# Kernel optimization log

Measured on AMD Instinct MI355X. Metric: run time of the kernel, lower is better.

Reference implementation:

```python
import jax, jax.numpy as jnp
import numpy as np

N, E = 20000, 5000
IN_FT, OUT_FT = 128, 128
DENSITY = 0.01  # fraction of nonzeros in the incidence matrix


def setup_inputs() -> dict:
    key = jax.random.key(0)
    kx, kh, kw, kb = jax.random.split(key, 4)
    X = jax.random.normal(kx, (N, IN_FT), dtype=jnp.float32)
    H = (jax.random.uniform(kh, (N, E)) < DENSITY).astype(jnp.float32)
    # xavier_normal_ with gain=0.01
    xav_std = 0.01 * np.sqrt(2.0 / (IN_FT + OUT_FT))
    weight_trans = jax.random.normal(kw, (IN_FT, OUT_FT), dtype=jnp.float32) * xav_std
    bias = jax.random.normal(kb, (OUT_FT,), dtype=jnp.float32) * 0.01
    return {"X": X, "H": H, "weight_trans": weight_trans, "bias": bias}


def reference(X, H, weight_trans, bias):
    # X: [N, in_ft], H: [N, E] incidence
    Xw = X @ weight_trans                      # [N, out_ft]
    DV = jnp.sum(H, axis=1) + 1e-12            # node degrees, [N]
    DE = jnp.sum(H, axis=0) + 1e-12            # hyperedge degrees, [E]
    # G = diag(1/DV) @ H @ diag(1/DE) @ H^T applied to Xw, computed in the
    # efficient order without materializing the NxN matrix G:
    M = H.T @ Xw                               # [E, out_ft]
    M = M / DE[:, None]                        # diag(1/DE) scaling
    out = H @ M                                # [N, out_ft]
    out = out / DV[:, None]                    # diag(1/DV) scaling
    out = out + bias
    return jax.nn.relu(out)
```

## Files before the change

kernel.cpp:

```cpp
#include <hip/hip_runtime.h>
#include <hip/hip_bf16.h>

#define N_NODES 20000
#define N_EDGES 5000
#define FT 128
#define CH_ROWS 320
#define N_CHUNKS 63
#define N_PANELS 79
#define SEG 24
#define SEG_STRIDE 1536
#define MAX_DEG 320

__global__ __launch_bounds__(256) void x_to_bf16(
    const float2* __restrict__ X2, __hip_bfloat162* __restrict__ Xb2) {
  int i = blockIdx.x * 256 + threadIdx.x;
  Xb2[i] = __float22bfloat162_rn(X2[i]);
}

__global__ __launch_bounds__(256) void scan_cols(
    const float* __restrict__ H,
    int* __restrict__ seg,
    int* __restrict__ scnt,
    unsigned long long* __restrict__ Hbt) {
  const int wid = threadIdx.x >> 6, lane = threadIdx.x & 63;
  const int panel = (blockIdx.x % 20) * 4 + wid;
  const int chunk = blockIdx.x / 20;
  if (panel >= N_PANELS) return;
  const int c = panel * 64 + lane;
  const bool cvalid = c < N_EDGES;
  const int r0 = chunk * CH_ROWS;
  const int rend = min(r0 + CH_ROWS, N_NODES);

  int* myseg = seg + c * SEG_STRIDE + chunk * SEG;
  unsigned long long* hb = Hbt + (size_t)panel * N_NODES;
  int cnt = 0;
  unsigned long long msk = 0ull;

  for (int rb = r0; rb < rend; rb += 8) {
    float v[8];
    const float* base = H + (size_t)rb * N_EDGES + c;
#pragma unroll
    for (int k = 0; k < 8; ++k) v[k] = 0.f;
    if (cvalid) {
#pragma unroll
      for (int k = 0; k < 8; ++k) v[k] = base[(size_t)k * N_EDGES];
    }
#pragma unroll
    for (int k = 0; k < 8; ++k) {
      int r = rb + k;
      unsigned long long bal = __ballot(v[k] != 0.f);
      msk = ((r & 63) == lane) ? bal : msk;
      if (((r & 63) == 63) || (r == N_NODES - 1)) {
        int g0 = r & ~63;
        if (g0 + lane < N_NODES) hb[g0 + lane] = msk;
        msk = 0ull;
      }
      if (v[k] != 0.f) {
        if (cnt < SEG) myseg[cnt] = r;
        ++cnt;
      }
    }
  }
  if (cvalid) scnt[c * 64 + chunk] = (cnt > SEG) ? SEG : cnt;
}

__global__ __launch_bounds__(256) void edge_gather(
    const __hip_bfloat162* __restrict__ Xb2,
    const int* __restrict__ seg, const int* __restrict__ scnt,
    float2* __restrict__ P2, int* __restrict__ de) {
  __shared__ int sidx[4][MAX_DEG];
  const int wid = threadIdx.x >> 6, lane = threadIdx.x & 63;
  const int e = blockIdx.x * 4 + wid;

  int cl = (lane < N_CHUNKS) ? scnt[e * 64 + lane] : 0;
  cl = min(cl, SEG);
  int off = cl;
  for (int d = 1; d < 64; d <<= 1) {
    int t = __shfl_up(off, d);
    if (lane >= d) off += t;
  }
  int total = __shfl(off, 63);
  off -= cl;
  if (cl > 0) {
    const int* sb = seg + e * SEG_STRIDE + lane * SEG;
    for (int i = 0; i < cl; ++i) {
      int o = off + i;
      if (o < MAX_DEG) sidx[wid][o] = sb[i];
    }
  }
  __builtin_amdgcn_s_waitcnt(0);
  int t = min(total, MAX_DEG);

  float sx = 0.f, sy = 0.f;
  int g = 0;
  for (; g + 8 <= t; g += 8) {
    int n0 = sidx[wid][g + 0], n1 = sidx[wid][g + 1];
    int n2 = sidx[wid][g + 2], n3 = sidx[wid][g + 3];
    int n4 = sidx[wid][g + 4], n5 = sidx[wid][g + 5];
    int n6 = sidx[wid][g + 6], n7 = sidx[wid][g + 7];
    float2 a0 = __bfloat1622float2(Xb2[n0 * 64 + lane]);
    float2 a1 = __bfloat1622float2(Xb2[n1 * 64 + lane]);
    float2 a2 = __bfloat1622float2(Xb2[n2 * 64 + lane]);
    float2 a3 = __bfloat1622float2(Xb2[n3 * 64 + lane]);
    float2 a4 = __bfloat1622float2(Xb2[n4 * 64 + lane]);
    float2 a5 = __bfloat1622float2(Xb2[n5 * 64 + lane]);
    float2 a6 = __bfloat1622float2(Xb2[n6 * 64 + lane]);
    float2 a7 = __bfloat1622float2(Xb2[n7 * 64 + lane]);
    sx += (a0.x + a1.x) + (a2.x + a3.x) + (a4.x + a5.x) + (a6.x + a7.x);
    sy += (a0.y + a1.y) + (a2.y + a3.y) + (a4.y + a5.y) + (a6.y + a7.y);
  }
  for (; g < t; ++g) {
    float2 a = __bfloat1622float2(Xb2[sidx[wid][g] * 64 + lane]);
    sx += a.x; sy += a.y;
  }
  P2[e * 64 + lane] = make_float2(sx, sy);
  if (lane == 0) de[e] = total;
}

__global__ __launch_bounds__(256) void gemm_M(
    const float* __restrict__ P, const float* __restrict__ W,
    const int* __restrict__ de, float* __restrict__ M) {
  int f = threadIdx.x & (FT - 1);
  int half = threadIdx.x >> 7;
  int base = blockIdx.x * 16 + half * 8;
#pragma unroll
  for (int g = 0; g < 8; g += 4) {
    int e = base + g;
    if (e >= N_EDGES) break;
    const float* p0 = P + (e + 0) * FT;
    const float* p1 = P + (e + 1) * FT;
    const float* p2 = P + (e + 2) * FT;
    const float* p3 = P + (e + 3) * FT;
    float a0 = 0.f, a1 = 0.f, a2 = 0.f, a3 = 0.f;
#pragma unroll 4
    for (int k = 0; k < FT; ++k) {
      float w = W[k * FT + f];
      a0 += p0[k] * w; a1 += p1[k] * w; a2 += p2[k] * w; a3 += p3[k] * w;
    }
    M[(e + 0) * FT + f] = a0 / ((float)de[e + 0] + 1e-12f);
    M[(e + 1) * FT + f] = a1 / ((float)de[e + 1] + 1e-12f);
    M[(e + 2) * FT + f] = a2 / ((float)de[e + 2] + 1e-12f);
    M[(e + 3) * FT + f] = a3 / ((float)de[e + 3] + 1e-12f);
  }
}

__global__ __launch_bounds__(256) void row_apply(
    const unsigned long long* __restrict__ Hbt,
    const float2* __restrict__ M2,
    const float2* __restrict__ bias2,
    float2* __restrict__ out2) {
  const int wid = threadIdx.x >> 6, lane = threadIdx.x & 63;
  const int n = blockIdx.x * 4 + wid;

  unsigned long long m0 = Hbt[(size_t)lane * N_NODES + n];
  unsigned long long m1 = (lane < N_PANELS - 64)
      ? Hbt[(size_t)(64 + lane) * N_NODES + n] : 0ull;
  float sx = 0.f, sy = 0.f;
  int dv = 0;
  for (int p = 0; p < N_PANELS; ++p) {
    unsigned long long mp = (p < 64) ? __shfl(m0, p) : __shfl(m1, p - 64);
    if (mp == 0ull) continue;
    dv += __popcll(mp);
    int ebase = p * 64;
    while (mp) {
      int b = __ffsll(mp) - 1;
      mp &= mp - 1;
      float2 mv = M2[(ebase + b) * 64 + lane];
      sx += mv.x; sy += mv.y;
    }
  }
  float inv = 1.f / ((float)dv + 1e-12f);
  float2 bb = bias2[lane];
  float2 o;
  o.x = fmaxf(fmaf(sx, inv, bb.x), 0.f);
  o.y = fmaxf(fmaf(sy, inv, bb.y), 0.f);
  out2[n * 64 + lane] = o;
}

extern "C" void kernel_launch(void* const* d_in, const int* in_sizes, int n_in,
                              void* d_out, int out_size, void* d_ws, size_t ws_size,
                              hipStream_t stream) {
  const float* X    = (const float*)d_in[0];
  const float* H    = (const float*)d_in[1];
  const float* W    = (const float*)d_in[2];
  const float* bias = (const float*)d_in[3];
  float* out = (float*)d_out;

  int* ws = (int*)d_ws;
  int* seg                 = ws;
  int* scnt                = ws + 7766016;
  unsigned long long* Hbt  = (unsigned long long*)(ws + 8089600);
  __hip_bfloat162* Xb2     = (__hip_bfloat162*)(ws + 11249600);
  float* P                 = (float*)(ws + 12529600);
  int* de                  = ws + 13169600;
  float* M                 = (float*)(ws + 13174720);

  x_to_bf16 <<<5000, 256, 0, stream>>>((const float2*)X, Xb2);
  scan_cols <<<20 * N_CHUNKS, 256, 0, stream>>>(H, seg, scnt, Hbt);
  edge_gather<<<N_EDGES / 4, 256, 0, stream>>>(Xb2, seg, scnt, (float2*)P, de);
  gemm_M    <<<(N_EDGES + 15) / 16, 256, 0, stream>>>(P, W, de, M);
  row_apply <<<N_NODES / 4, 256, 0, stream>>>(Hbt, (const float2*)M,
                                              (const float2*)bias, (float2*)out);
}
```

Before: 690.3 us.

## Scan H row-wise into interleaved bitmask, then build per-edge lists from bitmask

Replaces the column-strided scan of the dense incidence matrix with a row-wise float4 scan that ballots each row into an 80-word bitmask, using an interleaved edge-to-bit mapping (edge = 256*(vp/4) + 4*lane + vp%4). A separate list_build kernel then reads the compact bitmask to produce per-edge node segments with 32 chunks instead of 63. row_apply reads node-major bitmask rows contiguously. The intent is to turn the 400MB H read into fully coalesced vector loads and decouple list building from that read, at the cost of an extra kernel and a second pass over the bitmask.

```diff
diff --git a/kernel.cpp b/kernel.cpp
--- a/kernel.cpp
+++ b/kernel.cpp
@@ -4,11 +4,11 @@
 #define N_NODES 20000
 #define N_EDGES 5000
 #define FT 128
-#define CH_ROWS 320
-#define N_CHUNKS 63
-#define N_PANELS 79
+#define NVP 80
+#define ROW_U64 80
+#define N_CHUNKS 32
+#define CH_ROWS 625
 #define SEG 24
-#define SEG_STRIDE 1536
 #define MAX_DEG 320
 
 __global__ __launch_bounds__(256) void x_to_bf16(
@@ -17,51 +17,59 @@
   Xb2[i] = __float22bfloat162_rn(X2[i]);
 }
 
-__global__ __launch_bounds__(256) void scan_cols(
-    const float* __restrict__ H,
+__global__ __launch_bounds__(256) void scan_rows(
+    const float4* __restrict__ H4, unsigned long long* __restrict__ Hbt) {
+  const int wid = threadIdx.x >> 6, lane = threadIdx.x & 63;
+  const int r = blockIdx.x * 4 + wid;
+  const float4* base = H4 + (size_t)r * 1250;
+  unsigned long long m_lo = 0ull, m_hi = 0ull;
+#pragma unroll 4
+  for (int g = 0; g < 20; ++g) {
+    int idx4 = g * 64 + lane;
+    float4 v = make_float4(0.f, 0.f, 0.f, 0.f);
+    if (idx4 < 1250) v = base[idx4];
+    unsigned long long b0 = __ballot(v.x != 0.f);
+    unsigned long long b1 = __ballot(v.y != 0.f);
+    unsigned long long b2 = __ballot(v.z != 0.f);
+    unsigned long long b3 = __ballot(v.w != 0.f);
+    int vp = 4 * g;
+    if (vp < 64) {
+      m_lo = (lane == vp)     ? b0 : m_lo;
+      m_lo = (lane == vp + 1) ? b1 : m_lo;
+      m_lo = (lane == vp + 2) ? b2 : m_lo;
+      m_lo = (lane == vp + 3) ? b3 : m_lo;
+    } else {
+      m_hi = (lane == vp - 64) ? b0 : m_hi;
+      m_hi = (lane == vp - 63) ? b1 : m_hi;
+      m_hi = (lane == vp - 62) ? b2 : m_hi;
+      m_hi = (lane == vp - 61) ? b3 : m_hi;
+    }
+  }
+  Hbt[(size_t)r * ROW_U64 + lane] = m_lo;
+  if (lane < 16) Hbt[(size_t)r * ROW_U64 + 64 + lane] = m_hi;
+}
+
+__global__ __launch_bounds__(256) void list_build(
+    const unsigned long long* __restrict__ Hbt,
     int* __restrict__ seg,
-    int* __restrict__ scnt,
-    unsigned long long* __restrict__ Hbt) {
-  const int wid = threadIdx.x >> 6, lane = threadIdx.x & 63;
-  const int panel = (blockIdx.x % 20) * 4 + wid;
-  const int chunk = blockIdx.x / 20;
-  if (panel >= N_PANELS) return;
-  const int c = panel * 64 + lane;
-  const bool cvalid = c < N_EDGES;
+    int* __restrict__ scnt) {
+  const int wid = threadIdx.x >> 6, lane = threadIdx.x & 63;
+  const int gw = blockIdx.x * 4 + wid;
+  const int vp = gw % NVP;
+  const int chunk = gw / NVP;
+  const int e = (vp >> 2) * 256 + 4 * lane + (vp & 3);
+  int* myseg = seg + e * (N_CHUNKS * SEG) + chunk * SEG;
   const int r0 = chunk * CH_ROWS;
-  const int rend = min(r0 + CH_ROWS, N_NODES);
-
-  int* myseg = seg + c * SEG_STRIDE + chunk * SEG;
-  unsigned long long* hb = Hbt + (size_t)panel * N_NODES;
   int cnt = 0;
-  unsigned long long msk = 0ull;
-
-  for (int rb = r0; rb < rend; rb += 8) {
-    float v[8];
-    const float* base = H + (size_t)rb * N_EDGES + c;
-#pragma unroll
-    for (int k = 0; k < 8; ++k) v[k] = 0.f;
-    if (cvalid) {
-#pragma unroll
-      for (int k = 0; k < 8; ++k) v[k] = base[(size_t)k * N_EDGES];
-    }
-#pragma unroll
-    for (int k = 0; k < 8; ++k) {
-      int r = rb + k;
-      unsigned long long bal = __ballot(v[k] != 0.f);
-      msk = ((r & 63) == lane) ? bal : msk;
-      if (((r & 63) == 63) || (r == N_NODES - 1)) {
-        int g0 = r & ~63;
-        if (g0 + lane < N_NODES) hb[g0 + lane] = msk;
-        msk = 0ull;
-      }
-      if (v[k] != 0.f) {
-        if (cnt < SEG) myseg[cnt] = r;
-        ++cnt;
-      }
-    }
-  }
-  if (cvalid) scnt[c * 64 + chunk] = (cnt > SEG) ? SEG : cnt;
+#pragma unroll 5
+  for (int i = 0; i < CH_ROWS; ++i) {
+    unsigned long long mp = Hbt[(size_t)(r0 + i) * ROW_U64 + vp];
+    if ((mp >> lane) & 1ull) {
+      if (cnt < SEG) myseg[cnt] = r0 + i;
+      ++cnt;
+    }
+  }
+  scnt[e * N_CHUNKS + chunk] = (cnt > SEG) ? SEG : cnt;
 }
 
 __global__ __launch_bounds__(256) void edge_gather(
@@ -72,17 +80,17 @@
   const int wid = threadIdx.x >> 6, lane = threadIdx.x & 63;
   const int e = blockIdx.x * 4 + wid;
 
-  int cl = (lane < N_CHUNKS) ? scnt[e * 64 + lane] : 0;
+  int cl = (lane < N_CHUNKS) ? scnt[e * N_CHUNKS + lane] : 0;
   cl = min(cl, SEG);
   int off = cl;
   for (int d = 1; d < 64; d <<= 1) {
     int t = __shfl_up(off, d);
     if (lane >= d) off += t;
   }
-  int total = __shfl(off, 63);
+  int total = __shfl(off, N_CHUNKS - 1);
   off -= cl;
   if (cl > 0) {
-    const int* sb = seg + e * SEG_STRIDE + lane * SEG;
+    const int* sb = seg + e * (N_CHUNKS * SEG) + lane * SEG;
     for (int i = 0; i < cl; ++i) {
       int o = off + i;
       if (o < MAX_DEG) sidx[wid][o] = sb[i];
@@ -146,26 +154,23 @@
 
 __global__ __launch_bounds__(256) void row_apply(
     const unsigned long long* __restrict__ Hbt,
-    const float2* __restrict__ M2,
-    const float2* __restrict__ bias2,
+    const float2* __restrict__ M2, const float2* __restrict__ bias2,
     float2* __restrict__ out2) {
   const int wid = threadIdx.x >> 6, lane = threadIdx.x & 63;
   const int n = blockIdx.x * 4 + wid;
-
-  unsigned long long m0 = Hbt[(size_t)lane * N_NODES + n];
-  unsigned long long m1 = (lane < N_PANELS - 64)
-      ? Hbt[(size_t)(64 + lane) * N_NODES + n] : 0ull;
+  unsigned long long m_lo = Hbt[(size_t)n * ROW_U64 + lane];
+  unsigned long long m_hi = (lane < 16) ? Hbt[(size_t)n * ROW_U64 + 64 + lane] : 0ull;
   float sx = 0.f, sy = 0.f;
   int dv = 0;
-  for (int p = 0; p < N_PANELS; ++p) {
-    unsigned long long mp = (p < 64) ? __shfl(m0, p) : __shfl(m1, p - 64);
+  for (int vp = 0; vp < NVP; ++vp) {
+    unsigned long long mp = (vp < 64) ? __shfl(m_lo, vp) : __shfl(m_hi, vp - 64);
     if (mp == 0ull) continue;
     dv += __popcll(mp);
-    int ebase = p * 64;
+    int ebase = (vp >> 2) * 256 + (vp & 3);
     while (mp) {
-      int b = __ffsll(mp) - 1;
+      int b = __ffsll((unsigned long long)mp) - 1;
       mp &= mp - 1;
-      float2 mv = M2[(ebase + b) * 64 + lane];
+      float2 mv = M2[(size_t)(ebase + 4 * b) * 64 + lane];
       sx += mv.x; sy += mv.y;
     }
   }
@@ -174,7 +179,7 @@
   float2 o;
   o.x = fmaxf(fmaf(sx, inv, bb.x), 0.f);
   o.y = fmaxf(fmaf(sy, inv, bb.y), 0.f);
-  out2[n * 64 + lane] = o;
+  out2[(size_t)n * 64 + lane] = o;
 }
 
 extern "C" void kernel_launch(void* const* d_in, const int* in_sizes, int n_in,
@@ -187,18 +192,19 @@
   float* out = (float*)d_out;
 
   int* ws = (int*)d_ws;
-  int* seg                 = ws;
-  int* scnt                = ws + 7766016;
-  unsigned long long* Hbt  = (unsigned long long*)(ws + 8089600);
-  __hip_bfloat162* Xb2     = (__hip_bfloat162*)(ws + 11249600);
-  float* P                 = (float*)(ws + 12529600);
-  int* de                  = ws + 13169600;
-  float* M                 = (float*)(ws + 13174720);
-
-  x_to_bf16 <<<5000, 256, 0, stream>>>((const float2*)X, Xb2);
-  scan_cols <<<20 * N_CHUNKS, 256, 0, stream>>>(H, seg, scnt, Hbt);
-  edge_gather<<<N_EDGES / 4, 256, 0, stream>>>(Xb2, seg, scnt, (float2*)P, de);
-  gemm_M    <<<(N_EDGES + 15) / 16, 256, 0, stream>>>(P, W, de, M);
-  row_apply <<<N_NODES / 4, 256, 0, stream>>>(Hbt, (const float2*)M,
-                                              (const float2*)bias, (float2*)out);
-}
+  unsigned long long* Hbt = (unsigned long long*)ws;
+  __hip_bfloat162* Xb2    = (__hip_bfloat162*)(ws + 3200000);
+  int* seg                = ws + 4480000;
+  int* scnt               = ws + 8412160;
+  float* P                = (float*)(ws + 8576000);
+  int* de                 = ws + 9216000;
+  float* M                = (float*)(ws + 9221120);
+
+  x_to_bf16  <<<5000, 256, 0, stream>>>((const float2*)X, Xb2);
+  scan_rows  <<<5000, 256, 0, stream>>>((const float4*)H, Hbt);
+  list_build <<<640, 256, 0, stream>>>(Hbt, seg, scnt);
+  edge_gather<<<1250, 256, 0, stream>>>(Xb2, seg, scnt, (float2*)P, de);
+  gemm_M     <<<(N_EDGES + 15) / 16, 256, 0, stream>>>(P, W, de, M);
+  row_apply  <<<5000, 256, 0, stream>>>(Hbt, (const float2*)M,
+                                        (const float2*)bias, (float2*)out);
+}
```

Result: slower. 878.1 us (+27.2%).
